# Optimization experiments

Hardware: AMD Instinct MI355X
Metric: run time of the kernel (lower is better)

Reference implementation:

```python
import jax, jax.numpy as jnp
import numpy as np

N_USERS = 100000
N_ITEMS = 50000
N = N_USERS + N_ITEMS
D = 64
NNZ = 2000000
B = 16384
LAYERS = 3
HYPER_X = 0.5


def setup_inputs() -> dict:
    key = jax.random.key(0)
    ks = jax.random.split(key, 10)
    return {
        "emb_user": jax.random.uniform(ks[0], (N_USERS, D), jnp.float32, -1.0, 1.0),
        "emb_item": jax.random.uniform(ks[1], (N_ITEMS, D), jnp.float32, -1.0, 1.0),
        "w_user": jax.random.uniform(ks[2], (D, D), jnp.float32, -1.0, 1.0),
        "w_item": jax.random.uniform(ks[3], (D, D), jnp.float32, -1.0, 1.0),
        "xij_emb1": jnp.full((N_ITEMS, 1), 2.0, jnp.float32),
        "xij_emb0": jnp.full((N_ITEMS, 1), -2.0, jnp.float32),
        "g_val": jax.random.uniform(ks[4], (NNZ,), jnp.float32, 0.0, 0.1),
        "g_row": jax.random.randint(ks[5], (NNZ,), 0, N, jnp.int32),
        "g_col": jax.random.randint(ks[6], (NNZ,), 0, N, jnp.int32),
        "users": jax.random.randint(ks[7], (B,), 0, N_USERS, jnp.int32),
        "items": jax.random.randint(ks[8], (B,), 0, N_ITEMS, jnp.int32),
        "xij": jax.random.randint(ks[9], (B,), 0, 2, jnp.int32),
    }


def _spmm(row, col, val, x):
    # sparse COO @ dense: gather rows of x by col, scale, scatter-add by row
    return jax.ops.segment_sum(val[:, None] * x[col], row, num_segments=N)


def reference(emb_user, emb_item, w_user, w_item, xij_emb1, xij_emb0,
              g_val, g_row, g_col, users, items, xij):
    # --- computer(): LightGCN propagation with running sum -> mean ---
    e = jnp.concatenate([emb_user, emb_item], axis=0)  # [N, D]
    acc = e
    for _ in range(LAYERS):
        e = _spmm(g_row, g_col, g_val, e)
        acc = acc + e
    light = acc / (LAYERS + 1)
    all_users, all_items = light[:N_USERS], light[N_USERS:]

    # --- forward(users, items, xij) ---
    ue = all_users[users]                  # [B, D]
    ie = all_items[items]                  # [B, D]
    xij_emb = jnp.where(xij[:, None] > 0, xij_emb1[items], xij_emb0[items])  # [B, 1]
    ue = ue @ w_user.T                     # Linear, no bias
    ie = ie @ w_item.T
    hx = jnp.float32(HYPER_X)
    ue = jnp.concatenate(
        [(1.0 - hx) * jax.nn.softmax(ue, axis=1),
         jnp.full((ue.shape[0], 1), hx, dtype=ue.dtype)], axis=1)
    ie = jax.nn.sigmoid(jnp.concatenate([ie, xij_emb], axis=1))
    return jnp.sum(ue * ie, axis=1)        # gamma [B]
```

## Files before the change

kernel.cpp:

```cpp
#include <hip/hip_runtime.h>
#include <cstddef>

#define D 64
#define RPB 512
#define MAXB 512
#define PCHUNK 4096
#define PTHREADS 512
#define EPT (PCHUNK / PTHREADS)
#define TB 64

static __device__ __forceinline__ unsigned short f2b(float f) {
    unsigned u = __float_as_uint(f);
    return (unsigned short)((u + 0x7FFFu + ((u >> 16) & 1u)) >> 16);
}
static __device__ __forceinline__ float b2f(unsigned short h) {
    return __uint_as_float(((unsigned)h) << 16);
}

__global__ void convert_kernel(const float* __restrict__ eu, const float* __restrict__ ei,
                               unsigned short* __restrict__ e0, int nd_user, int nd_total) {
    int i = blockIdx.x * blockDim.x + threadIdx.x;
    int stride = gridDim.x * blockDim.x;
    int nq = nd_total >> 2, nqu = nd_user >> 2;
    for (int idx = i; idx < nq; idx += stride) {
        float4 v = (idx < nqu) ? ((const float4*)eu)[idx] : ((const float4*)ei)[idx - nqu];
        ushort4 o;
        o.x = f2b(v.x); o.y = f2b(v.y); o.z = f2b(v.z); o.w = f2b(v.w);
        ((ushort4*)e0)[idx] = o;
    }
}

__global__ void mark_kernel(const int* __restrict__ users, const int* __restrict__ items,
                            int* __restrict__ flags, int B, int n_users) {
    int i = blockIdx.x * blockDim.x + threadIdx.x;
    if (i < B) {
        flags[users[i]] = 1;
        flags[n_users + items[i]] = 1;
    }
}

__global__ __launch_bounds__(256)
void bucket_hist_kernel(const int* __restrict__ row, int* __restrict__ ghist,
                        int nnz, int nb) {
    __shared__ int h[MAXB];
    for (int b = threadIdx.x; b < nb; b += blockDim.x) h[b] = 0;
    __syncthreads();
    int i = blockIdx.x * blockDim.x + threadIdx.x;
    int stride = gridDim.x * blockDim.x;
    for (int e = i; e < nnz; e += stride) atomicAdd(&h[row[e] >> 9], 1);
    __syncthreads();
    for (int b = threadIdx.x; b < nb; b += blockDim.x)
        if (h[b]) atomicAdd(&ghist[b], h[b]);
}

__global__ __launch_bounds__(256)
void bucket_scan_kernel(const int* __restrict__ ghist, int* __restrict__ bofs,
                        int* __restrict__ gcur, int nb, int nnz) {
    __shared__ int part[256];
    int seg = (nb + 255) >> 8;
    int base = threadIdx.x * seg;
    int s = 0;
    for (int i = 0; i < seg; ++i)
        if (base + i < nb) s += ghist[base + i];
    part[threadIdx.x] = s;
    __syncthreads();
    for (int off = 1; off < 256; off <<= 1) {
        int t = (threadIdx.x >= (unsigned)off) ? part[threadIdx.x - off] : 0;
        __syncthreads();
        part[threadIdx.x] += t;
        __syncthreads();
    }
    int run = part[threadIdx.x] - s;
    for (int i = 0; i < seg; ++i) {
        int b = base + i;
        if (b < nb) {
            bofs[b] = run;
            gcur[b] = run;
            run += ghist[b];
        }
    }
    if (threadIdx.x == 0) bofs[nb] = nnz;
}

__global__ __launch_bounds__(PTHREADS)
void partition_kernel(const int* __restrict__ row, const int* __restrict__ col,
                      const float* __restrict__ val, int* __restrict__ gcur,
                      uint2* __restrict__ ep, int nnz, int nb) {
    __shared__ uint2 sorted[PCHUNK];
    __shared__ unsigned short bid[PCHUNK];
    __shared__ int hist[MAXB];
    __shared__ int sc[MAXB];
    __shared__ int lofs[MAXB];
    __shared__ int gofs[MAXB];
    __shared__ int lcur[MAXB];

    int tid  = threadIdx.x;
    int cbeg = blockIdx.x * PCHUNK;
    int cend = min(nnz, cbeg + PCHUNK);
    int cnt  = cend - cbeg;

    for (int b = tid; b < MAXB; b += PTHREADS) hist[b] = 0;
    __syncthreads();

    unsigned mykey[EPT];
    float    myval[EPT];
    int      mybkt[EPT];
    #pragma unroll
    for (int k = 0; k < EPT; ++k) {
        int e = cbeg + k * PTHREADS + tid;
        mybkt[k] = -1;
        if (e < cend) {
            int r = row[e];
            int b = r >> 9;
            mykey[k] = (((unsigned)r & 511u) << 18) | (unsigned)col[e];
            myval[k] = val[e];
            mybkt[k] = b;
            atomicAdd(&hist[b], 1);
        }
    }
    __syncthreads();

    int own = (tid < nb) ? hist[tid] : 0;
    sc[tid] = own;
    __syncthreads();
    for (int off = 1; off < MAXB; off <<= 1) {
        int t = (tid >= off) ? sc[tid - off] : 0;
        __syncthreads();
        sc[tid] += t;
        __syncthreads();
    }
    int excl = sc[tid] - own;
    if (tid < nb) {
        lofs[tid] = excl;
        lcur[tid] = excl;
        if (own) gofs[tid] = atomicAdd(&gcur[tid], own) - excl;
    }
    __syncthreads();

    #pragma unroll
    for (int k = 0; k < EPT; ++k) {
        int b = mybkt[k];
        if (b >= 0) {
            int p = atomicAdd(&lcur[b], 1);
            sorted[p] = make_uint2(mykey[k], __float_as_uint(myval[k]));
            bid[p] = (unsigned short)b;
        }
    }
    __syncthreads();

    for (int p = tid; p < cnt; p += PTHREADS)
        ep[p + gofs[bid[p]]] = sorted[p];
}

__global__ __launch_bounds__(PTHREADS)
void rowsort_kernel(const uint2* __restrict__ ep, const int* __restrict__ bofs,
                    uint2* __restrict__ ep2, int* __restrict__ ptr,
                    int n, int nnz) {
    __shared__ int hist[RPB];
    __shared__ int sc[RPB];
    __shared__ int cur[RPB];
    int b = blockIdx.x;
    int beg = bofs[b], end = bofs[b + 1];
    int tid = threadIdx.x;
    hist[tid] = 0;
    __syncthreads();
    for (int e = beg + tid; e < end; e += PTHREADS)
        atomicAdd(&hist[ep[e].x >> 18], 1);
    __syncthreads();
    int own = hist[tid];
    sc[tid] = own;
    __syncthreads();
    for (int off = 1; off < RPB; off <<= 1) {
        int t = (tid >= off) ? sc[tid - off] : 0;
        __syncthreads();
        sc[tid] += t;
        __syncthreads();
    }
    int excl = sc[tid] - own;
    cur[tid] = excl;
    int r = (b << 9) + tid;
    if (r < n) ptr[r] = beg + excl;
    if (b == 0 && tid == 0) ptr[n] = nnz;
    __syncthreads();
    for (int e = beg + tid; e < end; e += PTHREADS) {
        uint2 kv = ep[e];
        int rl = kv.x >> 18;
        int p = atomicAdd(&cur[rl], 1);
        ep2[beg + p] = kv;
    }
}

__global__ __launch_bounds__(256)
void spmm_bf16_kernel(const int* __restrict__ ptr, const uint2* __restrict__ ep,
                      const unsigned short* __restrict__ x,
                      const int* __restrict__ flags,
                      unsigned short* __restrict__ y, int n) {
    int lane = threadIdx.x & 63;
    int wid  = (blockIdx.x * blockDim.x + threadIdx.x) >> 6;
    int sub  = lane & 15;
    int rg   = lane >> 4;
    int r    = wid * 4 + rg;
    if (r >= n) return;
    if (flags && !flags[r]) return;

    int beg = ptr[r], end = ptr[r + 1];
    int klbase = lane & 48;
    float4 s = make_float4(0.f, 0.f, 0.f, 0.f);

    for (int base = beg; base < end; base += 16) {
        int m = min(16, end - base);
        uint2 kv = (sub < m) ? ep[base + sub] : make_uint2(0u, 0u);
        int   myc = kv.x & 0x3FFFF;
        float myv = __uint_as_float(kv.y);
        int k = 0;
        for (; k + 4 <= m; k += 4) {
            int   c0 = __shfl(myc, klbase + k);
            int   c1 = __shfl(myc, klbase + k + 1);
            int   c2 = __shfl(myc, klbase + k + 2);
            int   c3 = __shfl(myc, klbase + k + 3);
            float v0 = __shfl(myv, klbase + k);
            float v1 = __shfl(myv, klbase + k + 1);
            float v2 = __shfl(myv, klbase + k + 2);
            float v3 = __shfl(myv, klbase + k + 3);
            ushort4 h0 = ((const ushort4*)(x + ((size_t)c0 << 6)))[sub];
            ushort4 h1 = ((const ushort4*)(x + ((size_t)c1 << 6)))[sub];
            ushort4 h2 = ((const ushort4*)(x + ((size_t)c2 << 6)))[sub];
            ushort4 h3 = ((const ushort4*)(x + ((size_t)c3 << 6)))[sub];
            s.x = fmaf(v0, b2f(h0.x), s.x); s.y = fmaf(v0, b2f(h0.y), s.y);
            s.z = fmaf(v0, b2f(h0.z), s.z); s.w = fmaf(v0, b2f(h0.w), s.w);
            s.x = fmaf(v1, b2f(h1.x), s.x); s.y = fmaf(v1, b2f(h1.y), s.y);
            s.z = fmaf(v1, b2f(h1.z), s.z); s.w = fmaf(v1, b2f(h1.w), s.w);
            s.x = fmaf(v2, b2f(h2.x), s.x); s.y = fmaf(v2, b2f(h2.y), s.y);
            s.z = fmaf(v2, b2f(h2.z), s.z); s.w = fmaf(v2, b2f(h2.w), s.w);
            s.x = fmaf(v3, b2f(h3.x), s.x); s.y = fmaf(v3, b2f(h3.y), s.y);
            s.z = fmaf(v3, b2f(h3.z), s.z); s.w = fmaf(v3, b2f(h3.w), s.w);
        }
        for (; k < m; ++k) {
            int   c = __shfl(myc, klbase + k);
            float v = __shfl(myv, klbase + k);
            ushort4 h = ((const ushort4*)(x + ((size_t)c << 6)))[sub];
            s.x = fmaf(v, b2f(h.x), s.x); s.y = fmaf(v, b2f(h.y), s.y);
            s.z = fmaf(v, b2f(h.z), s.z); s.w = fmaf(v, b2f(h.w), s.w);
        }
    }

    ushort4 o;
    o.x = f2b(s.x); o.y = f2b(s.y); o.z = f2b(s.z); o.w = f2b(s.w);
    ((ushort4*)(y + ((size_t)r << 6)))[sub] = o;
}

__global__ __launch_bounds__(256)
void head_kernel(const float* __restrict__ eu, const float* __restrict__ ei,
                 const unsigned short* __restrict__ e1,
                 const unsigned short* __restrict__ e2,
                 const unsigned short* __restrict__ e3,
                 const float* __restrict__ wu, const float* __restrict__ wi,
                 const float* __restrict__ x1, const float* __restrict__ x0,
                 const int* __restrict__ users, const int* __restrict__ items,
                 const int* __restrict__ xij,
                 float* __restrict__ out, int B, int n_users) {
    __shared__ float uet[D * TB];
    __shared__ float iet[D * TB];
    __shared__ float wut[D * D];
    __shared__ float wit[D * D];

    int t  = threadIdx.x;
    int b0 = blockIdx.x * TB;

    for (int i = t; i < D * D; i += 256) {
        int k = i >> 6, j = i & 63;
        wut[i] = wu[j * D + k];
        wit[i] = wi[j * D + k];
    }

    {
        int l  = t & 15;
        int g  = t >> 4;
        for (int p = 0; p < 4; ++p) {
            int bl = g + p * 16;
            int b  = b0 + bl;
            if (b < B) {
                int u  = users[b];
                int it = items[b];
                size_t uo  = ((size_t)u << 6);
                size_t io  = ((size_t)(n_users + it) << 6);
                size_t io2 = ((size_t)it << 6);
                float4  fu = ((const float4*)(eu + uo))[l];
                ushort4 u1 = ((const ushort4*)(e1 + uo))[l];
                ushort4 u2 = ((const ushort4*)(e2 + uo))[l];
                ushort4 u3 = ((const ushort4*)(e3 + uo))[l];
                float4  fi = ((const float4*)(ei + io2))[l];
                ushort4 i1 = ((const ushort4*)(e1 + io))[l];
                ushort4 i2 = ((const ushort4*)(e2 + io))[l];
                ushort4 i3 = ((const ushort4*)(e3 + io))[l];
                int k0 = l << 2;
                uet[(k0 + 0) * TB + bl] = (fu.x + b2f(u1.x) + b2f(u2.x) + b2f(u3.x)) * 0.25f;
                uet[(k0 + 1) * TB + bl] = (fu.y + b2f(u1.y) + b2f(u2.y) + b2f(u3.y)) * 0.25f;
                uet[(k0 + 2) * TB + bl] = (fu.z + b2f(u1.z) + b2f(u2.z) + b2f(u3.z)) * 0.25f;
                uet[(k0 + 3) * TB + bl] = (fu.w + b2f(u1.w) + b2f(u2.w) + b2f(u3.w)) * 0.25f;
                iet[(k0 + 0) * TB + bl] = (fi.x + b2f(i1.x) + b2f(i2.x) + b2f(i3.x)) * 0.25f;
                iet[(k0 + 1) * TB + bl] = (fi.y + b2f(i1.y) + b2f(i2.y) + b2f(i3.y)) * 0.25f;
                iet[(k0 + 2) * TB + bl] = (fi.z + b2f(i1.z) + b2f(i2.z) + b2f(i3.z)) * 0.25f;
                iet[(k0 + 3) * TB + bl] = (fi.w + b2f(i1.w) + b2f(i2.w) + b2f(i3.w)) * 0.25f;
            }
        }
    }
    __syncthreads();

    int jg = (t & 15) << 2;
    int bg = (t >> 4) << 2;
    float su[4][4], si[4][4];
    #pragma unroll
    for (int a = 0; a < 4; ++a)
        #pragma unroll
        for (int c = 0; c < 4; ++c) { su[a][c] = 0.f; si[a][c] = 0.f; }

    #pragma unroll 4
    for (int k = 0; k < D; ++k) {
        float4 u4 = *(const float4*)&uet[k * TB + bg];
        float4 i4 = *(const float4*)&iet[k * TB + bg];
        float4 a4 = *(const float4*)&wut[k * D + jg];
        float4 c4 = *(const float4*)&wit[k * D + jg];
        const float ub[4] = {u4.x, u4.y, u4.z, u4.w};
        const float ib[4] = {i4.x, i4.y, i4.z, i4.w};
        const float wa[4] = {a4.x, a4.y, a4.z, a4.w};
        const float wc[4] = {c4.x, c4.y, c4.z, c4.w};
        #pragma unroll
        for (int a = 0; a < 4; ++a)
            #pragma unroll
            for (int c = 0; c < 4; ++c) {
                su[a][c] = fmaf(ub[a], wa[c], su[a][c]);
                si[a][c] = fmaf(ib[a], wc[c], si[a][c]);
            }
    }

    float m[4], S[4], T[4];
    #pragma unroll
    for (int a = 0; a < 4; ++a) {
        float mm = fmaxf(fmaxf(su[a][0], su[a][1]), fmaxf(su[a][2], su[a][3]));
        for (int off = 1; off < 16; off <<= 1) mm = fmaxf(mm, __shfl_xor(mm, off));
        m[a] = mm;
    }
    #pragma unroll
    for (int a = 0; a < 4; ++a) {
        float sl = 0.f, tl = 0.f;
        #pragma unroll
        for (int c = 0; c < 4; ++c) {
            float e = __expf(su[a][c] - m[a]);
            float g = 1.f / (1.f + __expf(-si[a][c]));
            sl += e;
            tl = fmaf(e, g, tl);
        }
        for (int off = 1; off < 16; off <<= 1) {
            sl += __shfl_xor(sl, off);
            tl += __shfl_xor(tl, off);
        }
        S[a] = sl; T[a] = tl;
    }

    if ((t & 15) == 0) {
        #pragma unroll
        for (int a = 0; a < 4; ++a) {
            int b = b0 + bg + a;
            if (b < B) {
                int it = items[b];
                float xe   = (xij[b] > 0) ? x1[it] : x0[it];
                float sigx = 1.f / (1.f + __expf(-xe));
                out[b] = 0.5f * T[a] / S[a] + 0.5f * sigx;
            }
        }
    }
}

__global__ void init_kernel(const float* __restrict__ eu, const float* __restrict__ ei,
                            float* __restrict__ e_cur, float* __restrict__ acc,
                            int nd_user, int nd_total) {
    int i = blockIdx.x * blockDim.x + threadIdx.x;
    int stride = gridDim.x * blockDim.x;
    int nq = nd_total >> 2;
    int nq_user = nd_user >> 2;
    for (int idx = i; idx < nq; idx += stride) {
        float4 v;
        if (idx < nq_user) v = ((const float4*)eu)[idx];
        else               v = ((const float4*)ei)[idx - nq_user];
        ((float4*)e_cur)[idx] = v;
        ((float4*)acc)[idx]   = v;
    }
}

__global__ void spmm_atomic_kernel(const int* __restrict__ row, const int* __restrict__ col,
                                   const float* __restrict__ val, const float* __restrict__ x,
                                   float* __restrict__ y, int nnz) {
    int lane  = threadIdx.x & 63;
    int wave  = (blockIdx.x * blockDim.x + threadIdx.x) >> 6;
    int nwave = (gridDim.x * blockDim.x) >> 6;
    for (int e = wave; e < nnz; e += nwave)
        atomicAdd(&y[(size_t)row[e] * D + lane], val[e] * x[(size_t)col[e] * D + lane]);
}

__global__ void accum_kernel(float* __restrict__ acc, const float* __restrict__ nxt,
                             int nd_total) {
    int i = blockIdx.x * blockDim.x + threadIdx.x;
    int stride = gridDim.x * blockDim.x;
    int nq = nd_total >> 2;
    for (int idx = i; idx < nq; idx += stride) {
        float4 a = ((float4*)acc)[idx];
        float4 b = ((const float4*)nxt)[idx];
        a.x += b.x; a.y += b.y; a.z += b.z; a.w += b.w;
        ((float4*)acc)[idx] = a;
    }
}

__global__ __launch_bounds__(256)
void head_acc_kernel(const float* __restrict__ acc,
                     const float* __restrict__ wu, const float* __restrict__ wi,
                     const float* __restrict__ x1, const float* __restrict__ x0,
                     const int* __restrict__ users, const int* __restrict__ items,
                     const int* __restrict__ xij,
                     float* __restrict__ out, int B, int n_users) {
    __shared__ float wtu[D * D];
    __shared__ float wti[D * D];
    for (int idx = threadIdx.x; idx < D * D; idx += blockDim.x) {
        int j = idx >> 6, k = idx & 63;
        wtu[k * D + j] = wu[idx];
        wti[k * D + j] = wi[idx];
    }
    __syncthreads();
    int lane = threadIdx.x & 63;
    int wid  = threadIdx.x >> 6;
    int nw   = blockDim.x >> 6;
    for (int b = blockIdx.x * nw + wid; b < B; b += gridDim.x * nw) {
        int u  = users[b];
        int it = items[b];
        float ue = acc[(size_t)u * D + lane] * 0.25f;
        float ie = acc[(size_t)(n_users + it) * D + lane] * 0.25f;
        float su = 0.f, si = 0.f;
        #pragma unroll 8
        for (int k = 0; k < D; ++k) {
            float uk = __shfl(ue, k);
            float ik = __shfl(ie, k);
            su = fmaf(uk, wtu[k * D + lane], su);
            si = fmaf(ik, wti[k * D + lane], si);
        }
        float m = su;
        for (int off = 32; off > 0; off >>= 1) m = fmaxf(m, __shfl_xor(m, off));
        float p = __expf(su - m);
        float sden = p;
        for (int off = 32; off > 0; off >>= 1) sden += __shfl_xor(sden, off);
        float soft = p / sden;
        float sig  = 1.f / (1.f + __expf(-si));
        float term = 0.5f * soft * sig;
        for (int off = 32; off > 0; off >>= 1) term += __shfl_xor(term, off);
        if (lane == 0) {
            float xe   = (xij[b] > 0) ? x1[it] : x0[it];
            float sigx = 1.f / (1.f + __expf(-xe));
            out[b] = term + 0.5f * sigx;
        }
    }
}

extern "C" void kernel_launch(void* const* d_in, const int* in_sizes, int n_in,
                              void* d_out, int out_size, void* d_ws, size_t ws_size,
                              hipStream_t stream) {
    const float* emb_user = (const float*)d_in[0];
    const float* emb_item = (const float*)d_in[1];
    const float* w_user   = (const float*)d_in[2];
    const float* w_item   = (const float*)d_in[3];
    const float* xij_emb1 = (const float*)d_in[4];
    const float* xij_emb0 = (const float*)d_in[5];
    const float* g_val    = (const float*)d_in[6];
    const int*   g_row    = (const int*)d_in[7];
    const int*   g_col    = (const int*)d_in[8];
    const int*   users    = (const int*)d_in[9];
    const int*   items    = (const int*)d_in[10];
    const int*   xij      = (const int*)d_in[11];
    float*       out      = (float*)d_out;

    const int n_users = in_sizes[0] / D;
    const int n_items = in_sizes[1] / D;
    const int n_total = n_users + n_items;
    const int nnz     = in_sizes[6];
    const int B       = in_sizes[9];

    const int nd_user  = n_users * D;
    const int nd_total = n_total * D;
    const int nb = (n_total + RPB - 1) / RPB;

    const size_t hbytes   = (((size_t)nd_total * 2) + 255) & ~(size_t)255;
    const size_t ebytes   = (size_t)nnz * sizeof(uint2);
    const size_t ptrbytes = ((size_t)(n_total + 1) * 4 + 255) & ~(size_t)255;
    const size_t flbytes  = ((size_t)n_total * 4 + 255) & ~(size_t)255;
    const size_t ibytes   = ((size_t)(nb + 1) * 4 + 255) & ~(size_t)255;
    const size_t need = 4 * hbytes + 2 * ebytes + ptrbytes + flbytes + 3 * ibytes + 256;

    if (ws_size >= need && nb <= MAXB) {
        char* w = (char*)d_ws;
        unsigned short* e0 = (unsigned short*)w;  w += hbytes;
        unsigned short* e1 = (unsigned short*)w;  w += hbytes;
        unsigned short* e2 = (unsigned short*)w;  w += hbytes;
        unsigned short* e3 = (unsigned short*)w;  w += hbytes;
        uint2* ep    = (uint2*)w;                 w += ebytes;
        uint2* ep2   = (uint2*)w;                 w += ebytes;
        int*   ptr   = (int*)w;                   w += ptrbytes;
        int*   flags = (int*)w;                   w += flbytes;
        int*   ghist = (int*)w;                   w += ibytes;
        int*   bofs  = (int*)w;                   w += ibytes;
        int*   gcur  = (int*)w;                   w += ibytes;

        hipMemsetAsync(ghist, 0, (size_t)nb * 4, stream);
        hipMemsetAsync(flags, 0, (size_t)n_total * 4, stream);

        convert_kernel<<<2048, 256, 0, stream>>>(emb_user, emb_item, e0,
                                                 nd_user, nd_total);
        mark_kernel<<<(B + 255) / 256, 256, 0, stream>>>(users, items, flags,
                                                         B, n_users);

        bucket_hist_kernel<<<256, 256, 0, stream>>>(g_row, ghist, nnz, nb);
        bucket_scan_kernel<<<1, 256, 0, stream>>>(ghist, bofs, gcur, nb, nnz);
        const int pblocks = (nnz + PCHUNK - 1) / PCHUNK;
        partition_kernel<<<pblocks, PTHREADS, 0, stream>>>(g_row, g_col, g_val, gcur,
                                                           ep, nnz, nb);
        rowsort_kernel<<<nb, PTHREADS, 0, stream>>>(ep, bofs, ep2, ptr, n_total, nnz);

        const int nblk = (n_total * 16 + 255) / 256;
        spmm_bf16_kernel<<<nblk, 256, 0, stream>>>(ptr, ep2, e0, nullptr, e1, n_total);
        spmm_bf16_kernel<<<nblk, 256, 0, stream>>>(ptr, ep2, e1, nullptr, e2, n_total);
        spmm_bf16_kernel<<<nblk, 256, 0, stream>>>(ptr, ep2, e2, flags,  e3, n_total);

        head_kernel<<<(B + TB - 1) / TB, 256, 0, stream>>>(
            emb_user, emb_item, e1, e2, e3,
            w_user, w_item, xij_emb1, xij_emb0,
            users, items, xij, out, B, n_users);
    } else {
        const size_t fbytes = (size_t)nd_total * sizeof(float);
        char* w = (char*)d_ws;
        float* e_a = (float*)w;  w += fbytes;
        float* e_b = (float*)w;  w += fbytes;
        float* acc = (float*)w;  w += fbytes;
        float* cur = e_a;
        float* nxt = e_b;
        init_kernel<<<2048, 256, 0, stream>>>(emb_user, emb_item, cur, acc,
                                              nd_user, nd_total);
        for (int l = 0; l < 3; ++l) {
            hipMemsetAsync(nxt, 0, fbytes, stream);
            spmm_atomic_kernel<<<2048, 256, 0, stream>>>(g_row, g_col, g_val, cur, nxt, nnz);
            accum_kernel<<<2048, 256, 0, stream>>>(acc, nxt, nd_total);
            float* t = cur; cur = nxt; nxt = t;
        }
        head_acc_kernel<<<256, 256, 0, stream>>>(acc, w_user, w_item,
                                                 xij_emb1, xij_emb0,
                                                 users, items, xij, out, B, n_users);
    }
}
```

Measured before the change: 293.2 us.

## Map one wavefront per row in bf16 SpMM with per-lane column

The SpMM kernel changes from four rows per wavefront (16 lanes per row, ushort4 gathers, shuffles to broadcast indices) to one row per 64-lane wavefront. Each lane owns one feature column, the edge list is read through uniform scalar-style loads, and each lane gathers one bf16 value per edge. This removes the shuffle overhead and improves load balance per row. In exchange it launches four times as many waves, and each lane issues 2-byte gathers instead of 8-byte vector gathers. Also removes an unused shared array in the partition kernel.

```diff
diff --git a/kernel.cpp b/kernel.cpp
--- a/kernel.cpp
+++ b/kernel.cpp
@@ -90,7 +90,6 @@
     __shared__ unsigned short bid[PCHUNK];
     __shared__ int hist[MAXB];
     __shared__ int sc[MAXB];
-    __shared__ int lofs[MAXB];
     __shared__ int gofs[MAXB];
     __shared__ int lcur[MAXB];
 
@@ -131,7 +130,6 @@
     }
     int excl = sc[tid] - own;
     if (tid < nb) {
-        lofs[tid] = excl;
         lcur[tid] = excl;
         if (own) gofs[tid] = atomicAdd(&gcur[tid], own) - excl;
     }
@@ -196,57 +194,39 @@
                       const int* __restrict__ flags,
                       unsigned short* __restrict__ y, int n) {
     int lane = threadIdx.x & 63;
-    int wid  = (blockIdx.x * blockDim.x + threadIdx.x) >> 6;
-    int sub  = lane & 15;
-    int rg   = lane >> 4;
-    int r    = wid * 4 + rg;
+    int r    = (blockIdx.x * blockDim.x + threadIdx.x) >> 6;
     if (r >= n) return;
     if (flags && !flags[r]) return;
 
-    int beg = ptr[r], end = ptr[r + 1];
-    int klbase = lane & 48;
-    float4 s = make_float4(0.f, 0.f, 0.f, 0.f);
-
-    for (int base = beg; base < end; base += 16) {
-        int m = min(16, end - base);
-        uint2 kv = (sub < m) ? ep[base + sub] : make_uint2(0u, 0u);
-        int   myc = kv.x & 0x3FFFF;
-        float myv = __uint_as_float(kv.y);
-        int k = 0;
-        for (; k + 4 <= m; k += 4) {
-            int   c0 = __shfl(myc, klbase + k);
-            int   c1 = __shfl(myc, klbase + k + 1);
-            int   c2 = __shfl(myc, klbase + k + 2);
-            int   c3 = __shfl(myc, klbase + k + 3);
-            float v0 = __shfl(myv, klbase + k);
-            float v1 = __shfl(myv, klbase + k + 1);
-            float v2 = __shfl(myv, klbase + k + 2);
-            float v3 = __shfl(myv, klbase + k + 3);
-            ushort4 h0 = ((const ushort4*)(x + ((size_t)c0 << 6)))[sub];
-            ushort4 h1 = ((const ushort4*)(x + ((size_t)c1 << 6)))[sub];
-            ushort4 h2 = ((const ushort4*)(x + ((size_t)c2 << 6)))[sub];
-            ushort4 h3 = ((const ushort4*)(x + ((size_t)c3 << 6)))[sub];
-            s.x = fmaf(v0, b2f(h0.x), s.x); s.y = fmaf(v0, b2f(h0.y), s.y);
-            s.z = fmaf(v0, b2f(h0.z), s.z); s.w = fmaf(v0, b2f(h0.w), s.w);
-            s.x = fmaf(v1, b2f(h1.x), s.x); s.y = fmaf(v1, b2f(h1.y), s.y);
-            s.z = fmaf(v1, b2f(h1.z), s.z); s.w = fmaf(v1, b2f(h1.w), s.w);
-            s.x = fmaf(v2, b2f(h2.x), s.x); s.y = fmaf(v2, b2f(h2.y), s.y);
-            s.z = fmaf(v2, b2f(h2.z), s.z); s.w = fmaf(v2, b2f(h2.w), s.w);
-            s.x = fmaf(v3, b2f(h3.x), s.x); s.y = fmaf(v3, b2f(h3.y), s.y);
-            s.z = fmaf(v3, b2f(h3.z), s.z); s.w = fmaf(v3, b2f(h3.w), s.w);
-        }
-        for (; k < m; ++k) {
-            int   c = __shfl(myc, klbase + k);
-            float v = __shfl(myv, klbase + k);
-            ushort4 h = ((const ushort4*)(x + ((size_t)c << 6)))[sub];
-            s.x = fmaf(v, b2f(h.x), s.x); s.y = fmaf(v, b2f(h.y), s.y);
-            s.z = fmaf(v, b2f(h.z), s.z); s.w = fmaf(v, b2f(h.w), s.w);
-        }
-    }
-
-    ushort4 o;
-    o.x = f2b(s.x); o.y = f2b(s.y); o.z = f2b(s.z); o.w = f2b(s.w);
-    ((ushort4*)(y + ((size_t)r << 6)))[sub] = o;
+    int beg = __builtin_amdgcn_readfirstlane(ptr[r]);
+    int end = __builtin_amdgcn_readfirstlane(ptr[r + 1]);
+    const uint2* __restrict__ e = ep + beg;
+    const unsigned short* __restrict__ xl = x + lane;
+    int deg = end - beg;
+
+    float acc = 0.f;
+    int j = 0;
+    for (; j + 4 <= deg; j += 4) {
+        uint2 k0 = e[j];
+        uint2 k1 = e[j + 1];
+        uint2 k2 = e[j + 2];
+        uint2 k3 = e[j + 3];
+        float x0 = b2f(xl[(size_t)(k0.x & 0x3FFFFu) << 6]);
+        float x1 = b2f(xl[(size_t)(k1.x & 0x3FFFFu) << 6]);
+        float x2 = b2f(xl[(size_t)(k2.x & 0x3FFFFu) << 6]);
+        float x3 = b2f(xl[(size_t)(k3.x & 0x3FFFFu) << 6]);
+        acc = fmaf(__uint_as_float(k0.y), x0, acc);
+        acc = fmaf(__uint_as_float(k1.y), x1, acc);
+        acc = fmaf(__uint_as_float(k2.y), x2, acc);
+        acc = fmaf(__uint_as_float(k3.y), x3, acc);
+    }
+    for (; j < deg; ++j) {
+        uint2 kv = e[j];
+        float xv = b2f(xl[(size_t)(kv.x & 0x3FFFFu) << 6]);
+        acc = fmaf(__uint_as_float(kv.y), xv, acc);
+    }
+
+    y[((size_t)r << 6) + lane] = f2b(acc);
 }
 
 __global__ __launch_bounds__(256)
@@ -347,9 +327,9 @@
         #pragma unroll
         for (int c = 0; c < 4; ++c) {
             float e = __expf(su[a][c] - m[a]);
-            float g = 1.f / (1.f + __expf(-si[a][c]));
+            float gg = 1.f / (1.f + __expf(-si[a][c]));
             sl += e;
-            tl = fmaf(e, g, tl);
+            tl = fmaf(e, gg, tl);
         }
         for (int off = 1; off < 16; off <<= 1) {
             sl += __shfl_xor(sl, off);
@@ -522,7 +502,7 @@
                                                            ep, nnz, nb);
         rowsort_kernel<<<nb, PTHREADS, 0, stream>>>(ep, bofs, ep2, ptr, n_total, nnz);
 
-        const int nblk = (n_total * 16 + 255) / 256;
+        const int nblk = (n_total * 64 + 255) / 256;
         spmm_bf16_kernel<<<nblk, 256, 0, stream>>>(ptr, ep2, e0, nullptr, e1, n_total);
         spmm_bf16_kernel<<<nblk, 256, 0, stream>>>(ptr, ep2, e1, nullptr, e2, n_total);
         spmm_bf16_kernel<<<nblk, 256, 0, stream>>>(ptr, ep2, e2, flags,  e3, n_total);
```

Measured after the change: 347.8 us. +18.6%, slower.
